# Kernel optimization log

Measured on AMD Instinct MI355X. Metric: run time of the kernel, lower is better.

The kernel has to match this reference:

```python
import jax, jax.numpy as jnp
import numpy as np

S = 2   # upsample scale
K = 5   # reassembly kernel k_up


def setup_inputs() -> dict:
    key = jax.random.key(0)
    ks = jax.random.split(key, 7)
    B, C, H, W = 4, 128, 64, 64
    C_MID = 64
    return {
        "x": jax.random.normal(ks[0], (B, C, H, W), dtype=jnp.float32),
        "w1": jax.random.normal(ks[1], (C_MID, C), dtype=jnp.float32) * 0.05,
        "w2": jax.random.normal(ks[2], (S * S * K * K, C_MID, 3, 3), dtype=jnp.float32) * 0.05,
        "bn_gamma": jax.random.uniform(ks[3], (C_MID,), dtype=jnp.float32, minval=0.5, maxval=1.5),
        "bn_beta": jax.random.normal(ks[4], (C_MID,), dtype=jnp.float32) * 0.1,
        "bn_mean": jax.random.normal(ks[5], (C_MID,), dtype=jnp.float32) * 0.1,
        "bn_var": jax.random.uniform(ks[6], (C_MID,), dtype=jnp.float32, minval=0.5, maxval=1.5),
    }


def reference(x, w1, w2, bn_gamma, bn_beta, bn_mean, bn_var):
    B, C, H, W = x.shape
    s, k = S, K
    eps = 1e-5
    # --- content encoder: 1x1 conv -> BN (inference form) -> ReLU -> 3x3 conv ---
    h = jnp.einsum('bchw,oc->bohw', x, w1)  # (B, c_mid, H, W)
    inv = bn_gamma / jnp.sqrt(bn_var + eps)
    h = h * inv[None, :, None, None] + (bn_beta - bn_mean * inv)[None, :, None, None]
    h = jax.nn.relu(h)
    ker = jax.lax.conv_general_dilated(
        h, w2, window_strides=(1, 1), padding=((1, 1), (1, 1)),
        dimension_numbers=('NCHW', 'OIHW', 'NCHW'))  # (B, s*s*k*k, H, W)
    # softmax over the k*k reassembly window
    ker = jax.nn.softmax(ker.reshape(B, s * s, k * k, H, W), axis=2)
    # --- unfold k x k neighborhoods of x (row-major window order, as F.unfold) ---
    p = k // 2
    xp = jnp.pad(x, ((0, 0), (0, 0), (p, p), (p, p)))
    patches = jnp.stack(
        [xp[:, :, i:i + H, j:j + W] for i in range(k) for j in range(k)],
        axis=2)  # (B, C, k*k, H, W)
    # weighted reassembly: sum over the k*k window per (sub-pixel, channel)
    out = jnp.einsum('bckhw,bskhw->bcshw', patches, ker)  # (B, C, s*s, H, W)
    # pixel shuffle: (B, C, s, s, H, W) -> (B, C, H*s, W*s)
    out = out.reshape(B, C, s, s, H, W).transpose(0, 1, 4, 2, 5, 3)
    return out.reshape(B, C, H * s, W * s)
```

## Files before the change

### kernel.cpp

```cpp
#include <hip/hip_runtime.h>
#include <hip/hip_bf16.h>

#define HW 4096
#define XSTR 100

typedef __attribute__((ext_vector_type(8))) short  short8;
typedef __attribute__((ext_vector_type(4))) float  floatx4;
typedef __attribute__((ext_vector_type(4))) unsigned short ushort4v;

#define OFF_W2B 0ul
#define OFF_W1B 129024ul
#define OFF_BN  145408ul
#define OFF_XG  145920ul
#define OFF_XPP 4340224ul

__global__ __launch_bounds__(256) void prep_kernel(const float* __restrict__ x,
                                                   const float* __restrict__ w1,
                                                   const float* __restrict__ w2,
                                                   const float* __restrict__ gamma,
                                                   const float* __restrict__ beta,
                                                   const float* __restrict__ mean,
                                                   const float* __restrict__ var,
                                                   char* __restrict__ ws) {
    int tid = blockIdx.x * 256 + threadIdx.x;
    if (tid < 262144) {
        int pix = tid & 4095;
        int cq  = (tid >> 12) & 15;
        int b   = tid >> 16;
        const float* xp = x + ((size_t)(b * 128 + cq * 8)) * HW + pix;
        union { short8 s; __hip_bfloat16 h[8]; } u;
        #pragma unroll
        for (int cc = 0; cc < 8; ++cc) u.h[cc] = __float2bfloat16(xp[(size_t)cc * HW]);
        *(short8*)((__hip_bfloat16*)(ws + OFF_XG) + (size_t)tid * 8) = u.s;
        return;
    }
    int t2 = tid - 262144;
    if (t2 < 64512) {
        int n = t2 / 576;
        int k = t2 - n * 576;
        int t = k >> 6, c = k & 63;
        float v = (n < 100) ? w2[(n * 64 + c) * 9 + t] : 0.f;
        ((__hip_bfloat16*)(ws + OFF_W2B))[t2] = __float2bfloat16(v);
    } else if (t2 < 64512 + 8192) {
        int i = t2 - 64512;
        ((__hip_bfloat16*)(ws + OFF_W1B))[i] = __float2bfloat16(w1[i]);
    } else if (t2 < 64512 + 8192 + 64) {
        int o = t2 - 64512 - 8192;
        float inv = gamma[o] * rsqrtf(var[o] + 1e-5f);
        ((float2*)(ws + OFF_BN))[o] = make_float2(inv, beta[o] - mean[o] * inv);
    } else {
        int t3 = t2 - 72768;
        if (t3 < 591872) {
            int j  = t3 % 17;
            int rr = t3 / 17;
            int row68 = rr - (rr / 68) * 68;
            int bc = rr / 68;
            int gy = row68 - 2;
            const float* xp = x + (size_t)bc * HW + (size_t)gy * 64;
            union { ushort4v u4; __hip_bfloat16 h[4]; } u;
            #pragma unroll
            for (int e = 0; e < 4; ++e) {
                int gx = j * 4 + e - 2;
                float f = 0.f;
                if ((unsigned)gy < 64u && (unsigned)gx < 64u) f = xp[gx];
                u.h[e] = __float2bfloat16(f);
            }
            *(ushort4v*)((__hip_bfloat16*)(ws + OFF_XPP) + (size_t)rr * 68 + j * 4) = u.u4;
        }
    }
}

__global__ __launch_bounds__(512, 4) void fused_carafe(const char* __restrict__ ws,
                                                       float* __restrict__ out) {
    __shared__ __align__(16) char smem[72960];
    __hip_bfloat16* xsT = (__hip_bfloat16*)smem;
    float*          lg  = (float*)(smem + 25600);
    __hip_bfloat16* hs  = (__hip_bfloat16*)(smem + 40192);
    __hip_bfloat16* whp = (__hip_bfloat16*)(smem + 40192);

    int b    = blockIdx.x >> 7;
    int tile = blockIdx.x & 127;
    int ty0 = (tile >> 3) * 4;
    int tx0 = (tile & 7) * 8;
    int tid = threadIdx.x;
    int lane = tid & 63, wave = tid >> 6;
    int q = lane >> 4, m = lane & 15;

    {
        const __hip_bfloat16* xpp = (const __hip_bfloat16*)(ws + OFF_XPP);
        #pragma unroll
        for (int it = 0; it < 2; ++it) {
            int idx = tid + it * 512;
            int c = idx >> 3, row = idx & 7;
            const __hip_bfloat16* src = xpp + (size_t)(b * 128 + c) * 4624
                                      + (size_t)(ty0 + row) * 68 + tx0;
            uint2 d0 = *(const uint2*)(src);
            uint2 d1 = *(const uint2*)(src + 4);
            uint2 d2 = *(const uint2*)(src + 8);
            __hip_bfloat16* dst = xsT + c * XSTR + row * 12;
            *(uint2*)(dst)     = d0;
            *(uint2*)(dst + 4) = d1;
            *(uint2*)(dst + 8) = d2;
        }
    }

    {
        const __hip_bfloat16* xg  = (const __hip_bfloat16*)(ws + OFF_XG) + (size_t)b * 16 * 4096 * 8;
        const __hip_bfloat16* w1b = (const __hip_bfloat16*)(ws + OFF_W1B);
        for (int task = wave; task < 16; task += 8) {
            int mt = task >> 2, nt = task & 3;
            int bo = nt * 16 + m;
            float2 bnia = ((const float2*)(ws + OFF_BN))[bo];
            int hp = mt * 16 + m;
            int hpc = (hp < 60) ? hp : 0;
            int hy1 = hpc / 10, hx1 = hpc - hy1 * 10;
            int gy = ty0 + hy1 - 1, gx = tx0 + hx1 - 1;
            int gyc = min(max(gy, 0), 63), gxc = min(max(gx, 0), 63);
            int pix = gyc * 64 + gxc;
            floatx4 acc;
            #pragma unroll
            for (int r = 0; r < 4; ++r) acc[r] = 0.f;
            #pragma unroll
            for (int s = 0; s < 4; ++s) {
                short8 a  = *(const short8*)(xg + ((size_t)((s * 4 + q) * 4096 + pix)) * 8);
                short8 bw = *(const short8*)(w1b + bo * 128 + s * 32 + q * 8);
                acc = __builtin_amdgcn_mfma_f32_16x16x32_bf16(a, bw, acc, 0, 0, 0);
            }
            #pragma unroll
            for (int r = 0; r < 4; ++r) {
                int prow = mt * 16 + q * 4 + r;
                if (prow < 60) {
                    int phy = prow / 10, phx = prow - phy * 10;
                    int gy2 = ty0 + phy - 1, gx2 = tx0 + phx - 1;
                    bool in = ((unsigned)gy2 < 64u) && ((unsigned)gx2 < 64u);
                    float v = in ? fmaxf(fmaf(acc[r], bnia.x, bnia.y), 0.f) : 0.f;
                    hs[prow * 64 + ((((bo >> 3) ^ (prow & 7)) << 3) | (bo & 7))] = __float2bfloat16(v);
                }
            }
        }
    }
    __syncthreads();

    {
        const __hip_bfloat16* w2b = (const __hip_bfloat16*)(ws + OFF_W2B);
        for (int task = wave; task < 14; task += 8) {
            int mt = task & 1, nt = task >> 1;
            int pixidx = mt * 16 + m;
            int py = pixidx >> 3, px = pixidx & 7;
            const __hip_bfloat16* bp = w2b + (size_t)(nt * 16 + m) * 576 + q * 8;

            floatx4 acc;
            #pragma unroll
            for (int r = 0; r < 4; ++r) acc[r] = 0.f;

            short8 bcur = *(const short8*)bp;
            for (int s = 0; s < 18; ++s) {
                int t = s >> 1, co = (s & 1) * 4 + q;
                int ti = t / 3, tj = t - ti * 3;
                int row = (py + ti) * 10 + (px + tj);
                short8 a = *(const short8*)(hs + row * 64 + ((co ^ (row & 7)) << 3));
                short8 bn2 = bcur;
                if (s < 17) bn2 = *(const short8*)(bp + (s + 1) * 32);
                acc = __builtin_amdgcn_mfma_f32_16x16x32_bf16(a, bcur, acc, 0, 0, 0);
                bcur = bn2;
            }
            #pragma unroll
            for (int r = 0; r < 4; ++r)
                lg[(mt * 16 + q * 4 + r) * 114 + nt * 16 + m] = acc[r];
        }
    }
    __syncthreads();

    {
        short8 z;
        #pragma unroll
        for (int j = 0; j < 8; ++j) z[j] = 0;
        char* wb = (char*)whp + tid * 64;
        #pragma unroll
        for (int j = 0; j < 4; ++j) *(short8*)(wb + j * 16) = z;
    }
    __syncthreads();

    {
        int row = tid >> 2, sub = tid & 3;
        int pixid = row >> 2, g = row & 3;
        int py = pixid >> 3, px = pixid & 7;
        int s = px >> 2, pxl = px & 3;
        int wrow = ((py << 2) | pxl) * 4 + g;
        float v[7];
        float mx = -1e30f;
        #pragma unroll
        for (int k = 0; k < 7; ++k) {
            int t25 = sub + k * 4;
            v[k] = (t25 < 25) ? lg[pixid * 114 + g * 25 + t25] : -1e30f;
            mx = fmaxf(mx, v[k]);
        }
        mx = fmaxf(mx, __shfl_xor(mx, 1, 64));
        mx = fmaxf(mx, __shfl_xor(mx, 2, 64));
        float ssum = 0.f;
        #pragma unroll
        for (int k = 0; k < 7; ++k) {
            int t25 = sub + k * 4;
            v[k] = (t25 < 25) ? __expf(v[k] - mx) : 0.f;
            ssum += v[k];
        }
        ssum += __shfl_xor(ssum, 1, 64);
        ssum += __shfl_xor(ssum, 2, 64);
        float rs = 1.f / ssum;
        #pragma unroll
        for (int k = 0; k < 7; ++k) {
            int t25 = sub + k * 4;
            if (t25 < 25) {
                int ti = t25 / 5, tj = t25 - ti * 5;
                int base = s * 8192 + wrow * 64
                         + ((((py + ti) ^ (wrow & 7)) << 3) | (pxl + tj));
                float kv = v[k] * rs;
                __hip_bfloat16 khi = __float2bfloat16(kv);
                whp[base] = khi;
                whp[base + 4096] = __float2bfloat16(kv - __bfloat162float(khi));
            }
        }
    }
    __syncthreads();

    {
        #pragma unroll
        for (int rep = 0; rep < 2; ++rep) {
            int task = wave + rep * 8;
            int s = task >> 3, ch = (task >> 2) & 1, pt = task & 3;
            const __hip_bfloat16* wbase = whp + s * 8192;
            int wrow = pt * 16 + m;
            int s0 = ((q ^ (wrow & 7)) << 3);
            int s1 = (((4 + q) ^ (wrow & 7)) << 3);
            short8 bh0 = *(const short8*)(wbase + wrow * 64 + s0);
            short8 bl0 = *(const short8*)(wbase + 4096 + wrow * 64 + s0);
            short8 bh1 = *(const short8*)(wbase + wrow * 64 + s1);
            short8 bl1 = *(const short8*)(wbase + 4096 + wrow * 64 + s1);

            int pxm = m >> 2, gy = (m >> 1) & 1, gx = m & 1;
            size_t rowoff = (size_t)(2 * (ty0 + pt) + gy) * 128
                          + 2 * (tx0 + s * 4 + pxm) + gx;

            #pragma unroll
            for (int ct = 0; ct < 4; ++ct) {
                int ca = ch * 64 + ct * 16 + m;
                const __hip_bfloat16* xr = xsT + ca * XSTR + s * 4;
                union { short8 v; uint2 d[2]; } a0u, a1u;
                a0u.d[0] = *(const uint2*)(xr + q * 12);
                a0u.d[1] = *(const uint2*)(xr + q * 12 + 4);
                a1u.d[0] = *(const uint2*)(xr + (4 + q) * 12);
                a1u.d[1] = *(const uint2*)(xr + (4 + q) * 12 + 4);
                floatx4 acc;
                #pragma unroll
                for (int r = 0; r < 4; ++r) acc[r] = 0.f;
                acc = __builtin_amdgcn_mfma_f32_16x16x32_bf16(a0u.v, bh0, acc, 0, 0, 0);
                acc = __builtin_amdgcn_mfma_f32_16x16x32_bf16(a0u.v, bl0, acc, 0, 0, 0);
                acc = __builtin_amdgcn_mfma_f32_16x16x32_bf16(a1u.v, bh1, acc, 0, 0, 0);
                acc = __builtin_amdgcn_mfma_f32_16x16x32_bf16(a1u.v, bl1, acc, 0, 0, 0);
                int cbase = ch * 64 + ct * 16 + q * 4;
                #pragma unroll
                for (int r = 0; r < 4; ++r)
                    out[(((size_t)(b * 128 + cbase + r)) << 14) + rowoff] = acc[r];
            }
        }
    }
}

extern "C" void kernel_launch(void* const* d_in, const int* in_sizes, int n_in,
                              void* d_out, int out_size, void* d_ws, size_t ws_size,
                              hipStream_t stream) {
    const float* x     = (const float*)d_in[0];
    const float* w1    = (const float*)d_in[1];
    const float* w2    = (const float*)d_in[2];
    const float* gamma = (const float*)d_in[3];
    const float* beta  = (const float*)d_in[4];
    const float* mean  = (const float*)d_in[5];
    const float* var   = (const float*)d_in[6];
    float* out = (float*)d_out;
    char*  ws  = (char*)d_ws;

    prep_kernel<<<3621, 256, 0, stream>>>(x, w1, w2, gamma, beta, mean, var, ws);
    fused_carafe<<<512, 512, 0, stream>>>(ws, out);
}
```

Baseline: 114.8 us.

## Stage reassembly outputs in LDS for float4 coalesced stores; prefetch w2 fragments

The final reassembly stage now writes MFMA results into a shared-memory staging buffer and then emits 16-byte float4 stores to global memory, in four phases with barriers in between. Before, each lane wrote scattered scalar floats. The w2 B-operand fragments in the 3x3 conv are preloaded nine at a time into registers with the loop fully unrolled. The zeroing of the weight buffer is moved earlier to drop one barrier. The cost is more LDS (80640 bytes per block, so fewer co-resident blocks), extra barriers, and higher register pressure.

```diff
diff --git a/kernel.cpp b/kernel.cpp
--- a/kernel.cpp
+++ b/kernel.cpp
@@ -72,11 +72,12 @@
 
 __global__ __launch_bounds__(512, 4) void fused_carafe(const char* __restrict__ ws,
                                                        float* __restrict__ out) {
-    __shared__ __align__(16) char smem[72960];
+    __shared__ __align__(16) char smem[80640];
     __hip_bfloat16* xsT = (__hip_bfloat16*)smem;
     float*          lg  = (float*)(smem + 25600);
+    float*          Dst = (float*)(smem + 25600);
     __hip_bfloat16* hs  = (__hip_bfloat16*)(smem + 40192);
-    __hip_bfloat16* whp = (__hip_bfloat16*)(smem + 40192);
+    __hip_bfloat16* whp = (__hip_bfloat16*)(smem + 47872);
 
     int b    = blockIdx.x >> 7;
     int tile = blockIdx.x & 127;
@@ -102,12 +103,20 @@
             *(uint2*)(dst + 4) = d1;
             *(uint2*)(dst + 8) = d2;
         }
+        short8 z;
+        #pragma unroll
+        for (int j = 0; j < 8; ++j) z[j] = 0;
+        char* wb = (char*)whp + tid * 64;
+        #pragma unroll
+        for (int j = 0; j < 4; ++j) *(short8*)(wb + j * 16) = z;
     }
 
     {
         const __hip_bfloat16* xg  = (const __hip_bfloat16*)(ws + OFF_XG) + (size_t)b * 16 * 4096 * 8;
         const __hip_bfloat16* w1b = (const __hip_bfloat16*)(ws + OFF_W1B);
-        for (int task = wave; task < 16; task += 8) {
+        #pragma unroll
+        for (int rep = 0; rep < 2; ++rep) {
+            int task = wave + rep * 8;
             int mt = task >> 2, nt = task & 3;
             int bo = nt * 16 + m;
             float2 bnia = ((const float2*)(ws + OFF_BN))[bo];
@@ -149,35 +158,27 @@
             int py = pixidx >> 3, px = pixidx & 7;
             const __hip_bfloat16* bp = w2b + (size_t)(nt * 16 + m) * 576 + q * 8;
 
+            short8 bv[9];
+            #pragma unroll
+            for (int s = 0; s < 9; ++s) bv[s] = *(const short8*)(bp + s * 32);
+
             floatx4 acc;
             #pragma unroll
             for (int r = 0; r < 4; ++r) acc[r] = 0.f;
 
-            short8 bcur = *(const short8*)bp;
+            #pragma unroll
             for (int s = 0; s < 18; ++s) {
                 int t = s >> 1, co = (s & 1) * 4 + q;
                 int ti = t / 3, tj = t - ti * 3;
                 int row = (py + ti) * 10 + (px + tj);
                 short8 a = *(const short8*)(hs + row * 64 + ((co ^ (row & 7)) << 3));
-                short8 bn2 = bcur;
-                if (s < 17) bn2 = *(const short8*)(bp + (s + 1) * 32);
-                acc = __builtin_amdgcn_mfma_f32_16x16x32_bf16(a, bcur, acc, 0, 0, 0);
-                bcur = bn2;
+                acc = __builtin_amdgcn_mfma_f32_16x16x32_bf16(a, bv[s % 9], acc, 0, 0, 0);
+                if (s < 9) bv[s] = *(const short8*)(bp + (s + 9) * 32);
             }
             #pragma unroll
             for (int r = 0; r < 4; ++r)
                 lg[(mt * 16 + q * 4 + r) * 114 + nt * 16 + m] = acc[r];
         }
-    }
-    __syncthreads();
-
-    {
-        short8 z;
-        #pragma unroll
-        for (int j = 0; j < 8; ++j) z[j] = 0;
-        char* wb = (char*)whp + tid * 64;
-        #pragma unroll
-        for (int j = 0; j < 4; ++j) *(short8*)(wb + j * 16) = z;
     }
     __syncthreads();
 
@@ -223,11 +224,12 @@
     }
     __syncthreads();
 
-    {
-        #pragma unroll
-        for (int rep = 0; rep < 2; ++rep) {
-            int task = wave + rep * 8;
-            int s = task >> 3, ch = (task >> 2) & 1, pt = task & 3;
+    #pragma unroll
+    for (int bb = 0; bb < 4; ++bb) {
+        const int s = bb >> 1, ptpair = bb & 1;
+        {
+            int ch = wave >> 2, ptloc = (wave >> 1) & 1, cthalf = wave & 1;
+            int pt = ptpair * 2 + ptloc;
             const __hip_bfloat16* wbase = whp + s * 8192;
             int wrow = pt * 16 + m;
             int s0 = ((q ^ (wrow & 7)) << 3);
@@ -236,13 +238,12 @@
             short8 bl0 = *(const short8*)(wbase + 4096 + wrow * 64 + s0);
             short8 bh1 = *(const short8*)(wbase + wrow * 64 + s1);
             short8 bl1 = *(const short8*)(wbase + 4096 + wrow * 64 + s1);
-
             int pxm = m >> 2, gy = (m >> 1) & 1, gx = m & 1;
-            size_t rowoff = (size_t)(2 * (ty0 + pt) + gy) * 128
-                          + 2 * (tx0 + s * 4 + pxm) + gx;
-
-            #pragma unroll
-            for (int ct = 0; ct < 4; ++ct) {
+            int rowsel = ptloc * 2 + gy;
+            int dcol = 2 * pxm + gx;
+            #pragma unroll
+            for (int ct2 = 0; ct2 < 2; ++ct2) {
+                int ct = cthalf * 2 + ct2;
                 int ca = ch * 64 + ct * 16 + m;
                 const __hip_bfloat16* xr = xsT + ca * XSTR + s * 4;
                 union { short8 v; uint2 d[2]; } a0u, a1u;
@@ -257,12 +258,28 @@
                 acc = __builtin_amdgcn_mfma_f32_16x16x32_bf16(a0u.v, bl0, acc, 0, 0, 0);
                 acc = __builtin_amdgcn_mfma_f32_16x16x32_bf16(a1u.v, bh1, acc, 0, 0, 0);
                 acc = __builtin_amdgcn_mfma_f32_16x16x32_bf16(a1u.v, bl1, acc, 0, 0, 0);
-                int cbase = ch * 64 + ct * 16 + q * 4;
+                int pbase = ch * 64 + ct * 16 + q * 4;
                 #pragma unroll
                 for (int r = 0; r < 4; ++r)
-                    out[(((size_t)(b * 128 + cbase + r)) << 14) + rowoff] = acc[r];
-            }
-        }
+                    Dst[(pbase + r) * 32 + rowsel * 8 + dcol] = acc[r];
+            }
+        }
+        __syncthreads();
+        {
+            #pragma unroll
+            for (int i = 0; i < 2; ++i) {
+                int unit = tid * 2 + i;
+                int plane = unit >> 3, rem = unit & 7;
+                int rowsel2 = rem >> 1, q4 = rem & 1;
+                const float* sp = Dst + plane * 32 + rowsel2 * 8 + q4 * 4;
+                float4 v = *(const float4*)sp;
+                int orow = 2 * (ty0 + ptpair * 2 + (rowsel2 >> 1)) + (rowsel2 & 1);
+                int ocol = 2 * (tx0 + s * 4) + q4 * 4;
+                *(float4*)(out + (((size_t)(b * 128 + plane)) << 14)
+                               + (size_t)orow * 128 + ocol) = v;
+            }
+        }
+        if (bb < 3) __syncthreads();
     }
 }
 
```

Result: no change. 115.5 us (+0.6%).
